# Performance work log

Measured on AMD Instinct MI355X. Metric: run time of the kernel, lower is better.

Reference implementation:

```python
import jax, jax.numpy as jnp
import numpy as np

B, T = 8, 32
D = 256                      # recurrent dim = 4*8*8 (product of embed dims)
SPEAKERS = 2
OUT_CELL = 64
N_CLASSES = 6
NUM_LAYERS = 2               # original shares ONE QRNNCell across layers ([cell]*num_layers)
BETA = 0.8                   # QActivation beta (scale_factor = 1)

def _unitary(rng, n):
    a = rng.normal(size=(n, n)) + 1j * rng.normal(size=(n, n))
    q, _ = np.linalg.qr(a)
    return jnp.asarray(q.real, jnp.float32), jnp.asarray(q.imag, jnp.float32)

def setup_inputs():
    key = jax.random.key(0)
    ks = jax.random.split(key, 18)
    rng = np.random.default_rng(0)
    def lin(k, fi, fo):
        kw, kb = jax.random.split(k)
        lim = 1.0 / np.sqrt(fi)
        return (jax.random.uniform(kw, (fi, fo), jnp.float32, -lim, lim),
                jax.random.uniform(kb, (fo,), jnp.float32, -lim, lim))
    Wt, bt = lin(ks[0], 300, 4)
    Wa, ba = lin(ks[1], 74, 8)
    Wv, bv = lin(ks[2], 35, 8)
    W1, b1 = lin(ks[3], D, OUT_CELL)
    W2, b2 = lin(ks[4], OUT_CELL, N_CLASSES)
    Ux_r, Ux_i = _unitary(rng, D)
    Uh_r, Uh_i = _unitary(rng, D)
    two_pi = float(2.0 * np.pi)
    return {
        'x_text': jax.random.normal(ks[5], (B, T, 300), jnp.float32),
        'x_audio': jax.random.normal(ks[6], (B, T, 74), jnp.float32),
        'x_video': jax.random.normal(ks[7], (B, T, 35), jnp.float32),
        'smask': jax.random.uniform(ks[8], (B, T, SPEAKERS), jnp.float32),
        'Wt': Wt, 'bt': bt, 'Wa': Wa, 'ba': ba, 'Wv': Wv, 'bv': bv,
        'Pt': jax.random.uniform(ks[9], (SPEAKERS, 4), jnp.float32, 0.0, two_pi),
        'Pa': jax.random.uniform(ks[10], (SPEAKERS, 8), jnp.float32, 0.0, two_pi),
        'Pv': jax.random.uniform(ks[11], (SPEAKERS, 8), jnp.float32, 0.0, two_pi),
        'Ux_r': Ux_r, 'Ux_i': Ux_i, 'Uh_r': Uh_r, 'Uh_i': Uh_i,
        'Lambda': jax.random.normal(ks[12], (), jnp.float32),
        'Kr': jax.random.normal(ks[13], (D, D), jnp.float32),
        'Ki': jax.random.normal(ks[14], (D, D), jnp.float32),
        'W1': W1, 'b1': b1, 'W2': W2, 'b2': b2,
    }

def _forward(x_text, x_audio, x_video, spk, Wt, bt, Wa, ba, Wv, bv, Pt, Pa, Pv,
             Ux_r, Ux_i, Uh_r, Uh_i, Lambda, Kr, Ki, W1, b1, W2, b2):
    def pure_state(x, W, b, P):
        r = jax.nn.relu(x @ W + b)
        amp = r / jnp.maximum(jnp.linalg.norm(r, axis=-1, keepdims=True), 1e-12)  # F.normalize
        ph = P[spk]                                   # (B,T,e) phase lookup by speaker id
        return amp * jnp.cos(ph), amp * jnp.sin(ph)   # ComplexMultiply
    tr_, ti_ = pure_state(x_text, Wt, bt, Pt)
    ar_, ai_ = pure_state(x_audio, Wa, ba, Pa)
    vr_, vi_ = pure_state(x_video, Wv, bv, Pv)
    def ckron(xr, xi, yr, yi):                        # QProduct: complex Kronecker product
        rr = jnp.einsum('bti,btj->btij', xr, yr) - jnp.einsum('bti,btj->btij', xi, yi)
        ii = jnp.einsum('bti,btj->btij', xr, yi) + jnp.einsum('bti,btj->btij', xi, yr)
        b_, t_ = rr.shape[:2]
        return rr.reshape(b_, t_, -1), ii.reshape(b_, t_, -1)
    pr, pi = ckron(tr_, ti_, ar_, ai_)
    pr, pi = ckron(pr, pi, vr_, vi_)                  # (B,T,D)
    # QOuter: rho = |psi><psi|, stored time-major for the scan
    rho_r = jnp.einsum('bti,btj->tbij', pr, pr) + jnp.einsum('bti,btj->tbij', pi, pi)
    rho_i = jnp.einsum('bti,btj->tbij', pi, pr) - jnp.einsum('bti,btj->tbij', pr, pi)
    lam = jax.nn.sigmoid(Lambda)
    eye = jnp.eye(D, dtype=pr.dtype) / D
    def evolve(Ur, Ui, rr, ri):                       # U rho U^dagger (complex, real/imag parts)
        Ar = jnp.einsum('pq,bqr->bpr', Ur, rr) - jnp.einsum('pq,bqr->bpr', Ui, ri)
        Ai = jnp.einsum('pq,bqr->bpr', Ur, ri) + jnp.einsum('pq,bqr->bpr', Ui, rr)
        Br = jnp.einsum('bpq,rq->bpr', Ar, Ur) + jnp.einsum('bpq,rq->bpr', Ai, Ui)
        Bi = jnp.einsum('bpq,rq->bpr', Ai, Ur) - jnp.einsum('bpq,rq->bpr', Ar, Ui)
        return Br, Bi
    def step(carry, x):                               # QRNNCell; activation only on emitted state
        hr, hi = carry
        xr, xi = x
        xer, xei = evolve(Ux_r, Ux_i, xr, xi)
        her, hei = evolve(Uh_r, Uh_i, hr, hi)
        nr = lam * xer + (1.0 - lam) * her
        ni = lam * xei + (1.0 - lam) * hei
        return (nr, ni), (BETA * nr + (1.0 - BETA) * eye, BETA * ni)  # QActivation (depolarize)
    xs = (rho_r, rho_i)
    for _ in range(NUM_LAYERS):                       # same (shared) cell each layer
        init = (jnp.broadcast_to(eye, rho_r.shape[1:]), jnp.zeros(rho_r.shape[1:], pr.dtype))
        _, xs = jax.lax.scan(step, init, xs)
    hr, hi = xs                                       # (T,B,D,D)
    # QMeasurement: p_k = Re <v_k| rho |v_k>, v_k L2-normalized complex vectors
    nrm = jnp.sqrt(jnp.sum(Kr * Kr + Ki * Ki, axis=-1, keepdims=True))
    mr, mi = Kr / nrm, Ki / nrm
    Prj_r = jnp.einsum('ki,kj->kij', mr, mr) + jnp.einsum('ki,kj->kij', mi, mi)
    Prj_i = jnp.einsum('ki,kj->kij', mr, mi) - jnp.einsum('ki,kj->kij', mi, mr)
    probs = jnp.einsum('tbij,kij->tbk', hr, Prj_r) - jnp.einsum('tbij,kij->tbk', hi, Prj_i)
    h1 = jax.nn.relu(probs @ W1 + b1)                 # SimpleNet (dropout = identity at eval)
    out = jnp.tanh(h1 @ W2 + b2)                      # (T,B,C)
    return jax.nn.log_softmax(jnp.moveaxis(out, 0, 1), axis=-1)  # (B,T,C)

def reference(x_text, x_audio, x_video, smask, Wt, bt, Wa, ba, Wv, bv, Pt, Pa, Pv,
              Ux_r, Ux_i, Uh_r, Uh_i, Lambda, Kr, Ki, W1, b1, W2, b2):
    spk = jnp.argmax(smask, axis=-1)
    return _forward(x_text, x_audio, x_video, spk, Wt, bt, Wa, ba, Wv, bv, Pt, Pa, Pv,
                    Ux_r, Ux_i, Uh_r, Uh_i, Lambda, Kr, Ki, W1, b1, W2, b2)
```

## Files before the change

kernel.cpp:

```cpp
#include <hip/hip_runtime.h>

#define TT 32
#define BETA_ 0.8f

typedef __bf16 bf16_t;
typedef bf16_t bf16x8 __attribute__((ext_vector_type(8)));
typedef float f32x4 __attribute__((ext_vector_type(4)));

#define PACC_F 256
#define BF_BASE_B 263168L
#define US 393216L
#define XU 131072L
#define XIB_E (76L * US)

#define LDSPAD 40

__device__ inline f32x4 MF(bf16x8 a, bf16x8 b, f32x4 c) {
    return __builtin_amdgcn_mfma_f32_16x16x32_bf16(a, b, c, 0, 0, 0);
}

__device__ inline void split6(float vr, float vi, bf16_t* o, long ps, long idx, int mask) {
    bf16_t rh = (bf16_t)vr; o[idx] = rh;
    bf16_t ih = (bf16_t)vi; o[ps + idx] = ih;
    if (mask & 1) {
        o[2*ps + idx] = (bf16_t)(vr - (float)rh);
        o[3*ps + idx] = (bf16_t)(vi - (float)ih);
    }
    if (mask & 2) {
        float nv = -vi; bf16_t nh = (bf16_t)nv;
        o[4*ps + idx] = nh;
        o[5*ps + idx] = (bf16_t)(nv - (float)nh);
    }
}

__global__ __launch_bounds__(256) void k_prep(
    const float* __restrict__ xt, const float* __restrict__ xa, const float* __restrict__ xv,
    const float* __restrict__ sm,
    const float* __restrict__ Wt, const float* __restrict__ bt,
    const float* __restrict__ Wa, const float* __restrict__ ba,
    const float* __restrict__ Wv, const float* __restrict__ bv,
    const float* __restrict__ Pt, const float* __restrict__ Pa, const float* __restrict__ Pv,
    const float* __restrict__ Uxr, const float* __restrict__ Uxi,
    const float* __restrict__ Uhr, const float* __restrict__ Uhi,
    const float* __restrict__ Lam, const float* __restrict__ Kr, const float* __restrict__ Ki,
    void* wsv)
{
    float* WF = (float*)wsv;
    bf16_t* bf = (bf16_t*)((char*)wsv + BF_BASE_B);
    const int blk = blockIdx.x, tid = threadIdx.x;
    __shared__ float red[256];
    __shared__ float rt[4], ra[8], rv[8], inv3[3];

    if (blk == 0) {
        if (tid != 0) return;
        float lam = 1.f / (1.f + expf(-Lam[0]));
        float oml = 1.f - lam;
        WF[0] = lam;
        WF[1] = BETA_ * BETA_ * lam * lam;
        float w = 1.f;
        for (int n = 0; n < 64; ++n) { WF[64 + n] = w; w *= oml; }
        float a1 = 1.f / 256.f, a2 = 1.f / 256.f;
        for (int t = 0; t < 32; ++t) {
            a1 = oml * a1;
            float y1 = BETA_ * a1 + (1.f - BETA_) / 256.f;
            a2 = lam * y1 + oml * a2;
            WF[8 + t] = BETA_ * a2 + (1.f - BETA_) / 256.f;
        }
        return;
    }
    if (blk < 513) {
        int i = (blk - 1) & 255, j = tid;
        if (blk < 257) {
            split6(Uxr[i * 256 + j], Uxi[i * 256 + j], bf + 0 * US, 65536L, (long)i * 256 + j, 3);
        } else {
            float vr = Uhr[i * 256 + j], vi = Uhi[i * 256 + j];
            split6(vr, vi, bf + 1 * US, 65536L, (long)i * 256 + j, 3);
            split6(vr, vi, bf + 2 * US, 65536L, (long)j * 256 + i, 3);
        }
        return;
    }
    if (blk < 769) {
        const int colS = blk - 513;
        const int t0 = colS >> 3, b = colS & 7;
        const long bt_ = (long)b * TT + t0;
        if (tid < 4) {
            float acc = bt[tid];
            const float* x = xt + bt_ * 300;
            for (int q = 0; q < 300; ++q) acc = fmaf(x[q], Wt[q * 4 + tid], acc);
            rt[tid] = fmaxf(acc, 0.f);
        } else if (tid < 12) {
            int u = tid - 4;
            float acc = ba[u];
            const float* x = xa + bt_ * 74;
            for (int q = 0; q < 74; ++q) acc = fmaf(x[q], Wa[q * 8 + u], acc);
            ra[u] = fmaxf(acc, 0.f);
        } else if (tid < 20) {
            int u = tid - 12;
            float acc = bv[u];
            const float* x = xv + bt_ * 35;
            for (int q = 0; q < 35; ++q) acc = fmaf(x[q], Wv[q * 8 + u], acc);
            rv[u] = fmaxf(acc, 0.f);
        }
        __syncthreads();
        if (tid == 0) {
            float s = 0.f; for (int u = 0; u < 4; ++u) s += rt[u] * rt[u];
            inv3[0] = 1.f / fmaxf(sqrtf(s), 1e-12f);
            s = 0.f; for (int u = 0; u < 8; ++u) s += ra[u] * ra[u];
            inv3[1] = 1.f / fmaxf(sqrtf(s), 1e-12f);
            s = 0.f; for (int u = 0; u < 8; ++u) s += rv[u] * rv[u];
            inv3[2] = 1.f / fmaxf(sqrtf(s), 1e-12f);
        }
        __syncthreads();
        float s0 = sm[bt_ * 2], s1 = sm[bt_ * 2 + 1];
        int spk = (s1 > s0) ? 1 : 0;
        int d = tid;
        int ti = d >> 6, ai = (d >> 3) & 7, vi = d & 7;
        float amp = (rt[ti] * inv3[0]) * (ra[ai] * inv3[1]) * (rv[vi] * inv3[2]);
        float ph = Pt[spk * 4 + ti] + Pa[spk * 8 + ai] + Pv[spk * 8 + vi];
        split6(amp * cosf(ph), amp * sinf(ph), bf + 3 * US, 65536L, (long)colS * 256 + d, 3);
        return;
    }
    {
        int k = blk - 769, i = tid;
        float vr = Kr[k * 256 + i], vi = Ki[k * 256 + i];
        red[i] = vr * vr + vi * vi;
        __syncthreads();
        for (int s = 128; s > 0; s >>= 1) { if (i < s) red[i] += red[i + s]; __syncthreads(); }
        float inv = 1.f / sqrtf(red[0]);
        split6(vr * inv, -vi * inv, bf + 44 * US, 65536L, (long)k * 256 + i, 3);
    }
}

struct Jobs {
    long aB[4], aS[4], bB[4], cB[4], cS[4];
    int wm[4], cnt[4];
};

__global__ __launch_bounds__(256) void k_gemm(void* wsv, Jobs J)
{
    bf16_t* bf = (bf16_t*)((char*)wsv + BF_BASE_B);
    int z = blockIdx.z, j = 0;
    while (z >= J.cnt[j]) { z -= J.cnt[j]; ++j; }
    const bf16_t* A = bf + J.aB[j] + (long)z * J.aS[j];
    const bf16_t* B = bf + J.bB[j];
    bf16_t*       C = bf + J.cB[j] + (long)z * J.cS[j];
    const int wmask = J.wm[j];

    __shared__ __align__(16) bf16_t sA[6][64][LDSPAD];
    __shared__ __align__(16) bf16_t sB[4][64][LDSPAD];
    const int m0 = blockIdx.x * 64, n0 = blockIdx.y * 64;
    const int tid = threadIdx.x;
    const int lane = tid & 63, w = tid >> 6;
    const int wm_ = w >> 1, wn = w & 1;
    const int fr = lane & 15, fg = lane >> 4;
    f32x4 accr[2][2] = {}; f32x4 acci[2][2] = {};
    for (int ks = 0; ks < 8; ++ks) {
        int idx = tid;
#pragma unroll
        for (int rep = 0; rep < 6; ++rep, idx += 256) {
            int p = idx >> 8, rem = idx & 255;
            int r = rem >> 2, cch = rem & 3;
            uint4 v = *(const uint4*)(A + (long)p * 65536 + (long)(m0 + r) * 256 + ks * 32 + cch * 8);
            *(uint4*)(&sA[p][r][cch * 8]) = v;
        }
        idx = tid;
#pragma unroll
        for (int rep = 0; rep < 4; ++rep, idx += 256) {
            int p = idx >> 8, rem = idx & 255;
            int r = rem >> 2, cch = rem & 3;
            uint4 v = *(const uint4*)(B + (long)p * 65536 + (long)(n0 + r) * 256 + ks * 32 + cch * 8);
            *(uint4*)(&sB[p][r][cch * 8]) = v;
        }
        __syncthreads();
        bf16x8 aF[2][6], bF[2][4];
#pragma unroll
        for (int fm = 0; fm < 2; ++fm) {
            int row = wm_ * 32 + fm * 16 + fr;
#pragma unroll
            for (int p = 0; p < 6; ++p) aF[fm][p] = *(const bf16x8*)(&sA[p][row][fg * 8]);
        }
#pragma unroll
        for (int fn = 0; fn < 2; ++fn) {
            int row = wn * 32 + fn * 16 + fr;
#pragma unroll
            for (int p = 0; p < 4; ++p) bF[fn][p] = *(const bf16x8*)(&sB[p][row][fg * 8]);
        }
#pragma unroll
        for (int fm = 0; fm < 2; ++fm)
#pragma unroll
            for (int fn = 0; fn < 2; ++fn) {
                f32x4 r = accr[fm][fn], im = acci[fm][fn];
                r  = MF(aF[fm][0], bF[fn][0], r );
                r  = MF(aF[fm][0], bF[fn][2], r );
                r  = MF(aF[fm][2], bF[fn][0], r );
                r  = MF(aF[fm][4], bF[fn][1], r );
                r  = MF(aF[fm][4], bF[fn][3], r );
                r  = MF(aF[fm][5], bF[fn][1], r );
                im = MF(aF[fm][0], bF[fn][1], im);
                im = MF(aF[fm][0], bF[fn][3], im);
                im = MF(aF[fm][2], bF[fn][1], im);
                im = MF(aF[fm][1], bF[fn][0], im);
                im = MF(aF[fm][1], bF[fn][2], im);
                im = MF(aF[fm][3], bF[fn][0], im);
                accr[fm][fn] = r; acci[fm][fn] = im;
            }
        __syncthreads();
    }
#pragma unroll
    for (int fm = 0; fm < 2; ++fm)
#pragma unroll
        for (int fn = 0; fn < 2; ++fn)
#pragma unroll
            for (int r4 = 0; r4 < 4; ++r4) {
                int m = m0 + wm_ * 32 + fm * 16 + fg * 4 + r4;
                int n = n0 + wn * 32 + fn * 16 + fr;
                split6(accr[fm][fn][r4], acci[fm][fn][r4], C, 65536L, (long)m * 256 + n, wmask);
            }
}

__global__ __launch_bounds__(256) void k_measure3(void* wsv)
{
    float* WF = (float*)wsv;
    bf16_t* bf = (bf16_t*)((char*)wsv + BF_BASE_B);
    const int t = blockIdx.z;
    const int cb = blockIdx.y;
    const int kblk = blockIdx.x >> 2, chunk = blockIdx.x & 3;
    const int cmax = t - 8 * chunk;
    const int clo = cb * 8;
    if (clo > cmax) return;
    const int chi = (clo + 8 < cmax + 1) ? clo + 8 : cmax + 1;

    __shared__ __align__(16) bf16_t sA[3][128][LDSPAD];
    __shared__ __align__(16) bf16_t sB[2][64][LDSPAD];
    __shared__ float part[128][9];
    const int tid = threadIdx.x;
    const int lane = tid & 63, w = tid >> 6;
    const int wm = w >> 1, wn = w & 1;
    const int fr = lane & 15, fg = lane >> 4;
    float sacc[4][2][4] = {};

    for (int c = clo; c < chi; ++c) {
        const int j0 = t - c;
        const bf16_t* H = bf + (long)(44 + c) * US;
        f32x4 accr[4][2] = {}; f32x4 acci[4][2] = {};
        for (int ks = 0; ks < 8; ++ks) {
            int idx = tid;
#pragma unroll
            for (int rep = 0; rep < 6; ++rep, idx += 256) {
                int p = idx >> 9, rem = idx & 511;
                int r = rem >> 2, cch = rem & 3;
                int pl = (p == 2) ? 4 : p;
                uint4 v = *(const uint4*)(H + (long)pl * 65536 + (long)(kblk * 128 + r) * 256 + ks * 32 + cch * 8);
                *(uint4*)(&sA[p][r][cch * 8]) = v;
            }
            idx = tid;
#pragma unroll
            for (int rep = 0; rep < 2; ++rep, idx += 256) {
                int p = idx >> 8, rem = idx & 255;
                int r = rem >> 2, cch = rem & 3;
                int t0g = chunk * 8 + (r >> 3);
                uint4 v = {0u, 0u, 0u, 0u};
                if (t0g <= j0) {
                    long base = XIB_E + (long)(j0 - t0g) * XU + (long)p * 65536
                              + (long)(chunk * 64 + r) * 256 + ks * 32 + cch * 8;
                    v = *(const uint4*)(bf + base);
                }
                *(uint4*)(&sB[p][r][cch * 8]) = v;
            }
            __syncthreads();
            bf16x8 aF[4][3], bF[2][2];
#pragma unroll
            for (int fm = 0; fm < 4; ++fm) {
                int row = wm * 64 + fm * 16 + fr;
#pragma unroll
                for (int p = 0; p < 3; ++p) aF[fm][p] = *(const bf16x8*)(&sA[p][row][fg * 8]);
            }
#pragma unroll
            for (int fn = 0; fn < 2; ++fn) {
                int row = wn * 32 + fn * 16 + fr;
#pragma unroll
                for (int p = 0; p < 2; ++p) bF[fn][p] = *(const bf16x8*)(&sB[p][row][fg * 8]);
            }
#pragma unroll
            for (int fm = 0; fm < 4; ++fm)
#pragma unroll
                for (int fn = 0; fn < 2; ++fn) {
                    f32x4 r = accr[fm][fn], im = acci[fm][fn];
                    r  = MF(aF[fm][0], bF[fn][0], r );
                    r  = MF(aF[fm][2], bF[fn][1], r );
                    im = MF(aF[fm][0], bF[fn][1], im);
                    im = MF(aF[fm][1], bF[fn][0], im);
                    accr[fm][fn] = r; acci[fm][fn] = im;
                }
            __syncthreads();
        }
#pragma unroll
        for (int fm = 0; fm < 4; ++fm)
#pragma unroll
            for (int fn = 0; fn < 2; ++fn)
#pragma unroll
                for (int r4 = 0; r4 < 4; ++r4) {
                    float vr = accr[fm][fn][r4], vi = acci[fm][fn][r4];
                    sacc[fm][fn][r4] += vr * vr + vi * vi;
                }
    }
    for (int e = tid; e < 128 * 9; e += 256) (&part[0][0])[e] = 0.f;
    __syncthreads();
#pragma unroll
    for (int fm = 0; fm < 4; ++fm)
#pragma unroll
        for (int fn = 0; fn < 2; ++fn)
#pragma unroll
            for (int r4 = 0; r4 < 4; ++r4) {
                int kl = wm * 64 + fm * 16 + fg * 4 + r4;
                int g = chunk * 64 + wn * 32 + fn * 16 + fr;
                int t0 = g >> 3;
                if (t0 <= t) atomicAdd(&part[kl][g & 7], WF[64 + (t - t0)] * sacc[fm][fn][r4]);
            }
    __syncthreads();
    float* pacc = WF + PACC_F;
    for (int e = tid; e < 1024; e += 256) {
        int kl = e >> 3, b = e & 7;
        float v = part[kl][b];
        if (v != 0.f) atomicAdd(&pacc[((t * 8 + b) << 8) + kblk * 128 + kl], v);
    }
}

__global__ __launch_bounds__(64) void k_mlp(
    const float* __restrict__ W1, const float* __restrict__ b1,
    const float* __restrict__ W2, const float* __restrict__ b2,
    const float* __restrict__ WF, float* __restrict__ out)
{
    const int t = blockIdx.x >> 3, b = blockIdx.x & 7;
    const int tid = threadIdx.x;
    __shared__ float pp[256], hh[64], oo[6];
    float ft = WF[8 + t], s2 = WF[1];
    const float* pacc = WF + PACC_F + ((t * 8 + b) << 8);
    for (int k = tid; k < 256; k += 64) pp[k] = ft + s2 * pacc[k];
    __syncthreads();
    float acc = b1[tid];
    for (int k = 0; k < 256; ++k) acc = fmaf(pp[k], W1[k * 64 + tid], acc);
    hh[tid] = fmaxf(acc, 0.f);
    __syncthreads();
    if (tid < 6) {
        float a = b2[tid];
        for (int k = 0; k < 64; ++k) a = fmaf(hh[k], W2[k * 6 + tid], a);
        oo[tid] = tanhf(a);
    }
    __syncthreads();
    if (tid == 0) {
        float m = oo[0];
        for (int c2 = 1; c2 < 6; ++c2) m = fmaxf(m, oo[c2]);
        float s = 0.f;
        for (int c2 = 0; c2 < 6; ++c2) s += expf(oo[c2] - m);
        float lse = m + logf(s);
        for (int c2 = 0; c2 < 6; ++c2) out[((long)b * 32 + t) * 6 + c2] = oo[c2] - lse;
    }
}

static inline void setJob(Jobs& J, int i, long aB, long aS, long bB, long cB, long cS,
                          int wm, int cnt)
{
    J.aB[i] = aB; J.aS[i] = aS; J.bB[i] = bB; J.cB[i] = cB; J.cS[i] = cS;
    J.wm[i] = wm; J.cnt[i] = cnt;
}

extern "C" void kernel_launch(void* const* d_in, const int* in_sizes, int n_in,
                              void* d_out, int out_size, void* d_ws, size_t ws_size,
                              hipStream_t stream)
{
    const float* xt  = (const float*)d_in[0];
    const float* xa  = (const float*)d_in[1];
    const float* xv  = (const float*)d_in[2];
    const float* sm  = (const float*)d_in[3];
    const float* Wt  = (const float*)d_in[4];
    const float* bt  = (const float*)d_in[5];
    const float* Wa  = (const float*)d_in[6];
    const float* ba  = (const float*)d_in[7];
    const float* Wv  = (const float*)d_in[8];
    const float* bv  = (const float*)d_in[9];
    const float* Pt  = (const float*)d_in[10];
    const float* Pa  = (const float*)d_in[11];
    const float* Pv  = (const float*)d_in[12];
    const float* Lam = (const float*)d_in[17];
    const float* Kr  = (const float*)d_in[18];
    const float* Ki  = (const float*)d_in[19];
    const float* W1  = (const float*)d_in[20];
    const float* b1  = (const float*)d_in[21];
    const float* W2  = (const float*)d_in[22];
    const float* b2  = (const float*)d_in[23];
    const float* Uxr = (const float*)d_in[13];
    const float* Uxi = (const float*)d_in[14];
    const float* Uhr = (const float*)d_in[15];
    const float* Uhi = (const float*)d_in[16];
    float* WF  = (float*)d_ws;
    float* out = (float*)d_out;

    hipMemsetAsync(WF + PACC_F, 0, 65536 * sizeof(float), stream);
    k_prep<<<1025, 256, 0, stream>>>(xt, xa, xv, sm, Wt, bt, Wa, ba, Wv, bv,
                                     Pt, Pa, Pv, Uxr, Uxi, Uhr, Uhi, Lam, Kr, Ki, d_ws);

    auto U = [](int u) { return (long)u * US; };
    dim3 blk(256);
    Jobs J;

    setJob(J, 0, U(1), 0, U(2), U(4), 0, 3, 1);
    setJob(J, 1, U(2), 0, U(1), U(5), 0, 3, 1);
    setJob(J, 2, U(3), 0, U(0), U(12), 0, 3, 1);
    setJob(J, 3, U(44), 0, U(2), U(45), 0, 3, 1);
    k_gemm<<<dim3(4, 4, 4), blk, 0, stream>>>(d_ws, J);
    setJob(J, 0, U(4), 0, U(5), U(6), 0, 3, 1);
    setJob(J, 1, U(5), 0, U(4), U(7), 0, 3, 1);
    setJob(J, 2, U(12), 0, U(1), U(13), 0, 3, 1);
    setJob(J, 3, U(44), US, U(5), U(46), US, 3, 2);
    k_gemm<<<dim3(4, 4, 5), blk, 0, stream>>>(d_ws, J);
    setJob(J, 0, U(6), 0, U(7), U(8), 0, 3, 1);
    setJob(J, 1, U(7), 0, U(6), U(9), 0, 3, 1);
    setJob(J, 2, U(12), US, U(4), U(14), US, 3, 2);
    setJob(J, 3, U(44), US, U(7), U(48), US, 3, 4);
    k_gemm<<<dim3(4, 4, 8), blk, 0, stream>>>(d_ws, J);
    setJob(J, 0, U(8), 0, U(9), U(10), 0, 3, 1);
    setJob(J, 1, U(9), 0, U(8), U(11), 0, 3, 1);
    setJob(J, 2, U(12), US, U(6), U(16), US, 3, 4);
    setJob(J, 3, U(44), US, U(9), U(52), US, 3, 8);
    k_gemm<<<dim3(4, 4, 14), blk, 0, stream>>>(d_ws, J);
    setJob(J, 0, U(12), US, U(8), U(20), US, 3, 8);
    setJob(J, 1, U(44), US, U(11), U(60), US, 3, 16);
    setJob(J, 2, 0, 0, 0, 0, 0, 0, 0);
    setJob(J, 3, 0, 0, 0, 0, 0, 0, 0);
    k_gemm<<<dim3(4, 4, 24), blk, 0, stream>>>(d_ws, J);
    setJob(J, 0, U(12), US, U(10), U(28), US, 3, 16);
    setJob(J, 1, U(12), US, U(0), XIB_E, XU, 0, 16);
    k_gemm<<<dim3(4, 4, 32), blk, 0, stream>>>(d_ws, J);
    setJob(J, 0, U(28), US, U(0), XIB_E + 16 * XU, XU, 0, 16);
    setJob(J, 1, 0, 0, 0, 0, 0, 0, 0);
    k_gemm<<<dim3(4, 4, 16), blk, 0, stream>>>(d_ws, J);

    k_measure3<<<dim3(8, 4, 32), blk, 0, stream>>>(d_ws);
    k_mlp<<<256, 64, 0, stream>>>(W1, b1, W2, b2, WF, out);
}
```

Before: 458.8 us.

## Drop stored negated-imag planes, split real accumulation, prefetch GEMM tiles, retile measure

The split-bf16 operand storage shrinks from six planes to four: the negated-imaginary planes are dropped, and the real part is built as the difference of two separate accumulators (positive and negative products). The GEMM kernel now prefetches the next k-slice into registers while computing the current one, and it uses a 'lo' mode with only hi planes (2 planes) for the final low-precision jobs. The measurement kernel is retiled into smaller 64x64 blocks with finer time-chunk skipping, giving more blocks. Together these cut memory traffic and LDS footprint and add latency hiding, at the cost of extra accumulator registers and the reworked indexing.

```diff
diff --git a/kernel.cpp b/kernel.cpp
--- a/kernel.cpp
+++ b/kernel.cpp
@@ -9,27 +9,20 @@
 
 #define PACC_F 256
 #define BF_BASE_B 263168L
-#define US 393216L
-#define XU 131072L
-#define XIB_E (76L * US)
-
-#define LDSPAD 40
+#define US4 262144L
+#define XU  131072L
+#define XIB_E (76L * US4)
 
 __device__ inline f32x4 MF(bf16x8 a, bf16x8 b, f32x4 c) {
     return __builtin_amdgcn_mfma_f32_16x16x32_bf16(a, b, c, 0, 0, 0);
 }
 
-__device__ inline void split6(float vr, float vi, bf16_t* o, long ps, long idx, int mask) {
+__device__ inline void splitW(float vr, float vi, bf16_t* o, long idx, int full) {
     bf16_t rh = (bf16_t)vr; o[idx] = rh;
-    bf16_t ih = (bf16_t)vi; o[ps + idx] = ih;
-    if (mask & 1) {
-        o[2*ps + idx] = (bf16_t)(vr - (float)rh);
-        o[3*ps + idx] = (bf16_t)(vi - (float)ih);
-    }
-    if (mask & 2) {
-        float nv = -vi; bf16_t nh = (bf16_t)nv;
-        o[4*ps + idx] = nh;
-        o[5*ps + idx] = (bf16_t)(nv - (float)nh);
+    bf16_t ih = (bf16_t)vi; o[65536L + idx] = ih;
+    if (full) {
+        o[2 * 65536L + idx] = (bf16_t)(vr - (float)rh);
+        o[3 * 65536L + idx] = (bf16_t)(vi - (float)ih);
     }
 }
 
@@ -71,11 +64,11 @@
     if (blk < 513) {
         int i = (blk - 1) & 255, j = tid;
         if (blk < 257) {
-            split6(Uxr[i * 256 + j], Uxi[i * 256 + j], bf + 0 * US, 65536L, (long)i * 256 + j, 3);
+            splitW(Uxr[i * 256 + j], Uxi[i * 256 + j], bf + 0 * US4, (long)i * 256 + j, 1);
         } else {
             float vr = Uhr[i * 256 + j], vi = Uhi[i * 256 + j];
-            split6(vr, vi, bf + 1 * US, 65536L, (long)i * 256 + j, 3);
-            split6(vr, vi, bf + 2 * US, 65536L, (long)j * 256 + i, 3);
+            splitW(vr, vi, bf + 1 * US4, (long)i * 256 + j, 1);
+            splitW(vr, vi, bf + 2 * US4, (long)j * 256 + i, 1);
         }
         return;
     }
@@ -117,7 +110,7 @@
         int ti = d >> 6, ai = (d >> 3) & 7, vi = d & 7;
         float amp = (rt[ti] * inv3[0]) * (ra[ai] * inv3[1]) * (rv[vi] * inv3[2]);
         float ph = Pt[spk * 4 + ti] + Pa[spk * 8 + ai] + Pv[spk * 8 + vi];
-        split6(amp * cosf(ph), amp * sinf(ph), bf + 3 * US, 65536L, (long)colS * 256 + d, 3);
+        splitW(amp * cosf(ph), amp * sinf(ph), bf + 3 * US4, (long)colS * 256 + d, 1);
         return;
     }
     {
@@ -127,16 +120,16 @@
         __syncthreads();
         for (int s = 128; s > 0; s >>= 1) { if (i < s) red[i] += red[i + s]; __syncthreads(); }
         float inv = 1.f / sqrtf(red[0]);
-        split6(vr * inv, -vi * inv, bf + 44 * US, 65536L, (long)k * 256 + i, 3);
+        splitW(vr * inv, -vi * inv, bf + 44 * US4, (long)k * 256 + i, 1);
     }
 }
 
 struct Jobs {
     long aB[4], aS[4], bB[4], cB[4], cS[4];
-    int wm[4], cnt[4];
+    int full[4], lo[4], cnt[4];
 };
 
-__global__ __launch_bounds__(256) void k_gemm(void* wsv, Jobs J)
+__global__ __launch_bounds__(256) void k_gemm2(void* wsv, Jobs J)
 {
     bf16_t* bf = (bf16_t*)((char*)wsv + BF_BASE_B);
     int z = blockIdx.z, j = 0;
@@ -144,136 +137,136 @@
     const bf16_t* A = bf + J.aB[j] + (long)z * J.aS[j];
     const bf16_t* B = bf + J.bB[j];
     bf16_t*       C = bf + J.cB[j] + (long)z * J.cS[j];
-    const int wmask = J.wm[j];
-
-    __shared__ __align__(16) bf16_t sA[6][64][LDSPAD];
-    __shared__ __align__(16) bf16_t sB[4][64][LDSPAD];
+    const int full = J.full[j], lo = J.lo[j];
+    const int nP = lo ? 2 : 4;
+
+    __shared__ __align__(16) bf16_t sA[4][64][40];
+    __shared__ __align__(16) bf16_t sB[4][64][40];
     const int m0 = blockIdx.x * 64, n0 = blockIdx.y * 64;
-    const int tid = threadIdx.x;
-    const int lane = tid & 63, w = tid >> 6;
-    const int wm_ = w >> 1, wn = w & 1;
-    const int fr = lane & 15, fg = lane >> 4;
-    f32x4 accr[2][2] = {}; f32x4 acci[2][2] = {};
-    for (int ks = 0; ks < 8; ++ks) {
-        int idx = tid;
-#pragma unroll
-        for (int rep = 0; rep < 6; ++rep, idx += 256) {
-            int p = idx >> 8, rem = idx & 255;
-            int r = rem >> 2, cch = rem & 3;
-            uint4 v = *(const uint4*)(A + (long)p * 65536 + (long)(m0 + r) * 256 + ks * 32 + cch * 8);
-            *(uint4*)(&sA[p][r][cch * 8]) = v;
-        }
-        idx = tid;
-#pragma unroll
-        for (int rep = 0; rep < 4; ++rep, idx += 256) {
-            int p = idx >> 8, rem = idx & 255;
-            int r = rem >> 2, cch = rem & 3;
-            uint4 v = *(const uint4*)(B + (long)p * 65536 + (long)(n0 + r) * 256 + ks * 32 + cch * 8);
-            *(uint4*)(&sB[p][r][cch * 8]) = v;
-        }
-        __syncthreads();
-        bf16x8 aF[2][6], bF[2][4];
-#pragma unroll
-        for (int fm = 0; fm < 2; ++fm) {
-            int row = wm_ * 32 + fm * 16 + fr;
-#pragma unroll
-            for (int p = 0; p < 6; ++p) aF[fm][p] = *(const bf16x8*)(&sA[p][row][fg * 8]);
-        }
-#pragma unroll
-        for (int fn = 0; fn < 2; ++fn) {
-            int row = wn * 32 + fn * 16 + fr;
-#pragma unroll
-            for (int p = 0; p < 4; ++p) bF[fn][p] = *(const bf16x8*)(&sB[p][row][fg * 8]);
-        }
-#pragma unroll
-        for (int fm = 0; fm < 2; ++fm)
-#pragma unroll
-            for (int fn = 0; fn < 2; ++fn) {
-                f32x4 r = accr[fm][fn], im = acci[fm][fn];
-                r  = MF(aF[fm][0], bF[fn][0], r );
-                r  = MF(aF[fm][0], bF[fn][2], r );
-                r  = MF(aF[fm][2], bF[fn][0], r );
-                r  = MF(aF[fm][4], bF[fn][1], r );
-                r  = MF(aF[fm][4], bF[fn][3], r );
-                r  = MF(aF[fm][5], bF[fn][1], r );
-                im = MF(aF[fm][0], bF[fn][1], im);
-                im = MF(aF[fm][0], bF[fn][3], im);
-                im = MF(aF[fm][2], bF[fn][1], im);
-                im = MF(aF[fm][1], bF[fn][0], im);
-                im = MF(aF[fm][1], bF[fn][2], im);
-                im = MF(aF[fm][3], bF[fn][0], im);
-                accr[fm][fn] = r; acci[fm][fn] = im;
-            }
-        __syncthreads();
-    }
-#pragma unroll
-    for (int fm = 0; fm < 2; ++fm)
-#pragma unroll
-        for (int fn = 0; fn < 2; ++fn)
-#pragma unroll
-            for (int r4 = 0; r4 < 4; ++r4) {
-                int m = m0 + wm_ * 32 + fm * 16 + fg * 4 + r4;
-                int n = n0 + wn * 32 + fn * 16 + fr;
-                split6(accr[fm][fn][r4], acci[fm][fn][r4], C, 65536L, (long)m * 256 + n, wmask);
-            }
-}
-
-__global__ __launch_bounds__(256) void k_measure3(void* wsv)
-{
-    float* WF = (float*)wsv;
-    bf16_t* bf = (bf16_t*)((char*)wsv + BF_BASE_B);
-    const int t = blockIdx.z;
-    const int cb = blockIdx.y;
-    const int kblk = blockIdx.x >> 2, chunk = blockIdx.x & 3;
-    const int cmax = t - 8 * chunk;
-    const int clo = cb * 8;
-    if (clo > cmax) return;
-    const int chi = (clo + 8 < cmax + 1) ? clo + 8 : cmax + 1;
-
-    __shared__ __align__(16) bf16_t sA[3][128][LDSPAD];
-    __shared__ __align__(16) bf16_t sB[2][64][LDSPAD];
-    __shared__ float part[128][9];
     const int tid = threadIdx.x;
     const int lane = tid & 63, w = tid >> 6;
     const int wm = w >> 1, wn = w & 1;
     const int fr = lane & 15, fg = lane >> 4;
-    float sacc[4][2][4] = {};
+    const int r_ = tid >> 2, cch = tid & 3;
+
+    f32x4 rp[2][2] = {}, rn[2][2] = {}, im[2][2] = {};
+    uint4 pa[4], pb[4];
+
+#pragma unroll
+    for (int p = 0; p < 4; ++p) if (p < nP) {
+        pa[p] = *(const uint4*)(A + (long)p * 65536 + (long)(m0 + r_) * 256 + cch * 8);
+        pb[p] = *(const uint4*)(B + (long)p * 65536 + (long)(n0 + r_) * 256 + cch * 8);
+    }
+    for (int ks = 0; ks < 8; ++ks) {
+        __syncthreads();
+#pragma unroll
+        for (int p = 0; p < 4; ++p) if (p < nP) {
+            *(uint4*)(&sA[p][r_][cch * 8]) = pa[p];
+            *(uint4*)(&sB[p][r_][cch * 8]) = pb[p];
+        }
+        __syncthreads();
+        if (ks < 7) {
+#pragma unroll
+            for (int p = 0; p < 4; ++p) if (p < nP) {
+                pa[p] = *(const uint4*)(A + (long)p * 65536 + (long)(m0 + r_) * 256 + (ks + 1) * 32 + cch * 8);
+                pb[p] = *(const uint4*)(B + (long)p * 65536 + (long)(n0 + r_) * 256 + (ks + 1) * 32 + cch * 8);
+            }
+        }
+        bf16x8 aF[2][4], bF[2][4];
+#pragma unroll
+        for (int fm = 0; fm < 2; ++fm) {
+            int row = wm * 32 + fm * 16 + fr;
+#pragma unroll
+            for (int p = 0; p < 4; ++p) if (p < nP) aF[fm][p] = *(const bf16x8*)(&sA[p][row][fg * 8]);
+        }
+#pragma unroll
+        for (int fn = 0; fn < 2; ++fn) {
+            int row = wn * 32 + fn * 16 + fr;
+#pragma unroll
+            for (int p = 0; p < 4; ++p) if (p < nP) bF[fn][p] = *(const bf16x8*)(&sB[p][row][fg * 8]);
+        }
+#pragma unroll
+        for (int fm = 0; fm < 2; ++fm)
+#pragma unroll
+            for (int fn = 0; fn < 2; ++fn) {
+                f32x4 p_ = rp[fm][fn], n_ = rn[fm][fn], i_ = im[fm][fn];
+                p_ = MF(aF[fm][0], bF[fn][0], p_);
+                n_ = MF(aF[fm][1], bF[fn][1], n_);
+                i_ = MF(aF[fm][0], bF[fn][1], i_);
+                i_ = MF(aF[fm][1], bF[fn][0], i_);
+                if (!lo) {
+                    p_ = MF(aF[fm][0], bF[fn][2], p_);
+                    p_ = MF(aF[fm][2], bF[fn][0], p_);
+                    n_ = MF(aF[fm][1], bF[fn][3], n_);
+                    n_ = MF(aF[fm][3], bF[fn][1], n_);
+                    i_ = MF(aF[fm][0], bF[fn][3], i_);
+                    i_ = MF(aF[fm][2], bF[fn][1], i_);
+                    i_ = MF(aF[fm][1], bF[fn][2], i_);
+                    i_ = MF(aF[fm][3], bF[fn][0], i_);
+                }
+                rp[fm][fn] = p_; rn[fm][fn] = n_; im[fm][fn] = i_;
+            }
+    }
+#pragma unroll
+    for (int fm = 0; fm < 2; ++fm)
+#pragma unroll
+        for (int fn = 0; fn < 2; ++fn)
+#pragma unroll
+            for (int r4 = 0; r4 < 4; ++r4) {
+                int m = m0 + wm * 32 + fm * 16 + fg * 4 + r4;
+                int n = n0 + wn * 32 + fn * 16 + fr;
+                float vr = rp[fm][fn][r4] - rn[fm][fn][r4];
+                splitW(vr, im[fm][fn][r4], C, (long)m * 256 + n, full);
+            }
+}
+
+__global__ __launch_bounds__(256) void k_measure4(void* wsv)
+{
+    float* WF = (float*)wsv;
+    bf16_t* bf = (bf16_t*)((char*)wsv + BF_BASE_B);
+    const int t = blockIdx.z;
+    const int clo = blockIdx.y * 4;
+    if (clo > t) return;
+    const int kblk = blockIdx.x >> 2, colc = blockIdx.x & 3;
+    if (colc * 8 > t - clo) return;
+    const int chi = (clo + 4 < t + 1) ? clo + 4 : t + 1;
+    const int k0 = kblk * 64;
+
+    __shared__ __align__(16) bf16_t sA[2][64][40];
+    __shared__ __align__(16) bf16_t sB[2][64][40];
+    __shared__ float part[64][9];
+    const int tid = threadIdx.x;
+    const int lane = tid & 63, w = tid >> 6;
+    const int wm = w >> 1, wn = w & 1;
+    const int fr = lane & 15, fg = lane >> 4;
+    const int r_ = tid >> 2, cch = tid & 3;
+    float sacc[2][2][4] = {};
+
+    const int t0r = colc * 8 + (r_ >> 3);
+    const long xrow = (long)(t0r * 8 + (r_ & 7)) * 256;
 
     for (int c = clo; c < chi; ++c) {
-        const int j0 = t - c;
-        const bf16_t* H = bf + (long)(44 + c) * US;
-        f32x4 accr[4][2] = {}; f32x4 acci[4][2] = {};
+        const bf16_t* H = bf + (44L + c) * US4;
+        const int av = t - c - t0r;
+        f32x4 rp[2][2] = {}, rn[2][2] = {}, im[2][2] = {};
         for (int ks = 0; ks < 8; ++ks) {
-            int idx = tid;
-#pragma unroll
-            for (int rep = 0; rep < 6; ++rep, idx += 256) {
-                int p = idx >> 9, rem = idx & 511;
-                int r = rem >> 2, cch = rem & 3;
-                int pl = (p == 2) ? 4 : p;
-                uint4 v = *(const uint4*)(H + (long)pl * 65536 + (long)(kblk * 128 + r) * 256 + ks * 32 + cch * 8);
-                *(uint4*)(&sA[p][r][cch * 8]) = v;
-            }
-            idx = tid;
-#pragma unroll
-            for (int rep = 0; rep < 2; ++rep, idx += 256) {
-                int p = idx >> 8, rem = idx & 255;
-                int r = rem >> 2, cch = rem & 3;
-                int t0g = chunk * 8 + (r >> 3);
+            __syncthreads();
+#pragma unroll
+            for (int p = 0; p < 2; ++p) {
+                *(uint4*)(&sA[p][r_][cch * 8]) =
+                    *(const uint4*)(H + (long)p * 65536 + (long)(k0 + r_) * 256 + ks * 32 + cch * 8);
                 uint4 v = {0u, 0u, 0u, 0u};
-                if (t0g <= j0) {
-                    long base = XIB_E + (long)(j0 - t0g) * XU + (long)p * 65536
-                              + (long)(chunk * 64 + r) * 256 + ks * 32 + cch * 8;
-                    v = *(const uint4*)(bf + base);
-                }
-                *(uint4*)(&sB[p][r][cch * 8]) = v;
+                if (av >= 0)
+                    v = *(const uint4*)(bf + XIB_E + (long)av * XU + (long)p * 65536 + xrow + ks * 32 + cch * 8);
+                *(uint4*)(&sB[p][r_][cch * 8]) = v;
             }
             __syncthreads();
-            bf16x8 aF[4][3], bF[2][2];
-#pragma unroll
-            for (int fm = 0; fm < 4; ++fm) {
-                int row = wm * 64 + fm * 16 + fr;
-#pragma unroll
-                for (int p = 0; p < 3; ++p) aF[fm][p] = *(const bf16x8*)(&sA[p][row][fg * 8]);
+            bf16x8 aF[2][2], bF[2][2];
+#pragma unroll
+            for (int fm = 0; fm < 2; ++fm) {
+                int row = wm * 32 + fm * 16 + fr;
+#pragma unroll
+                for (int p = 0; p < 2; ++p) aF[fm][p] = *(const bf16x8*)(&sA[p][row][fg * 8]);
             }
 #pragma unroll
             for (int fn = 0; fn < 2; ++fn) {
@@ -282,47 +275,47 @@
                 for (int p = 0; p < 2; ++p) bF[fn][p] = *(const bf16x8*)(&sB[p][row][fg * 8]);
             }
 #pragma unroll
-            for (int fm = 0; fm < 4; ++fm)
+            for (int fm = 0; fm < 2; ++fm)
 #pragma unroll
                 for (int fn = 0; fn < 2; ++fn) {
-                    f32x4 r = accr[fm][fn], im = acci[fm][fn];
-                    r  = MF(aF[fm][0], bF[fn][0], r );
-                    r  = MF(aF[fm][2], bF[fn][1], r );
-                    im = MF(aF[fm][0], bF[fn][1], im);
-                    im = MF(aF[fm][1], bF[fn][0], im);
-                    accr[fm][fn] = r; acci[fm][fn] = im;
+                    f32x4 p_ = rp[fm][fn], n_ = rn[fm][fn], i_ = im[fm][fn];
+                    p_ = MF(aF[fm][0], bF[fn][0], p_);
+                    n_ = MF(aF[fm][1], bF[fn][1], n_);
+                    i_ = MF(aF[fm][0], bF[fn][1], i_);
+                    i_ = MF(aF[fm][1], bF[fn][0], i_);
+                    rp[fm][fn] = p_; rn[fm][fn] = n_; im[fm][fn] = i_;
                 }
-            __syncthreads();
-        }
-#pragma unroll
-        for (int fm = 0; fm < 4; ++fm)
+        }
+#pragma unroll
+        for (int fm = 0; fm < 2; ++fm)
 #pragma unroll
             for (int fn = 0; fn < 2; ++fn)
 #pragma unroll
                 for (int r4 = 0; r4 < 4; ++r4) {
-                    float vr = accr[fm][fn][r4], vi = acci[fm][fn][r4];
+                    float vr = rp[fm][fn][r4] - rn[fm][fn][r4];
+                    float vi = im[fm][fn][r4];
                     sacc[fm][fn][r4] += vr * vr + vi * vi;
                 }
     }
-    for (int e = tid; e < 128 * 9; e += 256) (&part[0][0])[e] = 0.f;
+    for (int e = tid; e < 64 * 9; e += 256) (&part[0][0])[e] = 0.f;
     __syncthreads();
 #pragma unroll
-    for (int fm = 0; fm < 4; ++fm)
+    for (int fm = 0; fm < 2; ++fm)
 #pragma unroll
         for (int fn = 0; fn < 2; ++fn)
 #pragma unroll
             for (int r4 = 0; r4 < 4; ++r4) {
-                int kl = wm * 64 + fm * 16 + fg * 4 + r4;
-                int g = chunk * 64 + wn * 32 + fn * 16 + fr;
-                int t0 = g >> 3;
-                if (t0 <= t) atomicAdd(&part[kl][g & 7], WF[64 + (t - t0)] * sacc[fm][fn][r4]);
+                int kl = wm * 32 + fm * 16 + fg * 4 + r4;
+                int g = wn * 32 + fn * 16 + fr;
+                int t0 = colc * 8 + (g >> 3);
+                if (t0 <= t) atomicAdd(&part[kl][g & 7], WF[64 + t - t0] * sacc[fm][fn][r4]);
             }
     __syncthreads();
     float* pacc = WF + PACC_F;
-    for (int e = tid; e < 1024; e += 256) {
+    for (int e = tid; e < 512; e += 256) {
         int kl = e >> 3, b = e & 7;
         float v = part[kl][b];
-        if (v != 0.f) atomicAdd(&pacc[((t * 8 + b) << 8) + kblk * 128 + kl], v);
+        if (v != 0.f) atomicAdd(&pacc[((t * 8 + b) << 8) + k0 + kl], v);
     }
 }
 
@@ -359,10 +352,10 @@
 }
 
 static inline void setJob(Jobs& J, int i, long aB, long aS, long bB, long cB, long cS,
-                          int wm, int cnt)
+                          int full, int lo, int cnt)
 {
     J.aB[i] = aB; J.aS[i] = aS; J.bB[i] = bB; J.cB[i] = cB; J.cS[i] = cS;
-    J.wm[i] = wm; J.cnt[i] = cnt;
+    J.full[i] = full; J.lo[i] = lo; J.cnt[i] = cnt;
 }
 
 extern "C" void kernel_launch(void* const* d_in, const int* in_sizes, int n_in,
@@ -382,6 +375,10 @@
     const float* Pt  = (const float*)d_in[10];
     const float* Pa  = (const float*)d_in[11];
     const float* Pv  = (const float*)d_in[12];
+    const float* Uxr = (const float*)d_in[13];
+    const float* Uxi = (const float*)d_in[14];
+    const float* Uhr = (const float*)d_in[15];
+    const float* Uhi = (const float*)d_in[16];
     const float* Lam = (const float*)d_in[17];
     const float* Kr  = (const float*)d_in[18];
     const float* Ki  = (const float*)d_in[19];
@@ -389,10 +386,6 @@
     const float* b1  = (const float*)d_in[21];
     const float* W2  = (const float*)d_in[22];
     const float* b2  = (const float*)d_in[23];
-    const float* Uxr = (const float*)d_in[13];
-    const float* Uxi = (const float*)d_in[14];
-    const float* Uhr = (const float*)d_in[15];
-    const float* Uhi = (const float*)d_in[16];
     float* WF  = (float*)d_ws;
     float* out = (float*)d_out;
 
@@ -400,42 +393,42 @@
     k_prep<<<1025, 256, 0, stream>>>(xt, xa, xv, sm, Wt, bt, Wa, ba, Wv, bv,
                                      Pt, Pa, Pv, Uxr, Uxi, Uhr, Uhi, Lam, Kr, Ki, d_ws);
 
-    auto U = [](int u) { return (long)u * US; };
+    auto U = [](int u) { return (long)u * US4; };
     dim3 blk(256);
     Jobs J;
 
-    setJob(J, 0, U(1), 0, U(2), U(4), 0, 3, 1);
-    setJob(J, 1, U(2), 0, U(1), U(5), 0, 3, 1);
-    setJob(J, 2, U(3), 0, U(0), U(12), 0, 3, 1);
-    setJob(J, 3, U(44), 0, U(2), U(45), 0, 3, 1);
-    k_gemm<<<dim3(4, 4, 4), blk, 0, stream>>>(d_ws, J);
-    setJob(J, 0, U(4), 0, U(5), U(6), 0, 3, 1);
-    setJob(J, 1, U(5), 0, U(4), U(7), 0, 3, 1);
-    setJob(J, 2, U(12), 0, U(1), U(13), 0, 3, 1);
-    setJob(J, 3, U(44), US, U(5), U(46), US, 3, 2);
-    k_gemm<<<dim3(4, 4, 5), blk, 0, stream>>>(d_ws, J);
-    setJob(J, 0, U(6), 0, U(7), U(8), 0, 3, 1);
-    setJob(J, 1, U(7), 0, U(6), U(9), 0, 3, 1);
-    setJob(J, 2, U(12), US, U(4), U(14), US, 3, 2);
-    setJob(J, 3, U(44), US, U(7), U(48), US, 3, 4);
-    k_gemm<<<dim3(4, 4, 8), blk, 0, stream>>>(d_ws, J);
-    setJob(J, 0, U(8), 0, U(9), U(10), 0, 3, 1);
-    setJob(J, 1, U(9), 0, U(8), U(11), 0, 3, 1);
-    setJob(J, 2, U(12), US, U(6), U(16), US, 3, 4);
-    setJob(J, 3, U(44), US, U(9), U(52), US, 3, 8);
-    k_gemm<<<dim3(4, 4, 14), blk, 0, stream>>>(d_ws, J);
-    setJob(J, 0, U(12), US, U(8), U(20), US, 3, 8);
-    setJob(J, 1, U(44), US, U(11), U(60), US, 3, 16);
-    setJob(J, 2, 0, 0, 0, 0, 0, 0, 0);
-    setJob(J, 3, 0, 0, 0, 0, 0, 0, 0);
-    k_gemm<<<dim3(4, 4, 24), blk, 0, stream>>>(d_ws, J);
-    setJob(J, 0, U(12), US, U(10), U(28), US, 3, 16);
-    setJob(J, 1, U(12), US, U(0), XIB_E, XU, 0, 16);
-    k_gemm<<<dim3(4, 4, 32), blk, 0, stream>>>(d_ws, J);
-    setJob(J, 0, U(28), US, U(0), XIB_E + 16 * XU, XU, 0, 16);
-    setJob(J, 1, 0, 0, 0, 0, 0, 0, 0);
-    k_gemm<<<dim3(4, 4, 16), blk, 0, stream>>>(d_ws, J);
-
-    k_measure3<<<dim3(8, 4, 32), blk, 0, stream>>>(d_ws);
+    setJob(J, 0, U(1), 0, U(2), U(4), 0, 1, 0, 1);
+    setJob(J, 1, U(2), 0, U(1), U(5), 0, 1, 0, 1);
+    setJob(J, 2, U(3), 0, U(0), U(12), 0, 1, 0, 1);
+    setJob(J, 3, U(44), 0, U(2), U(45), 0, 1, 0, 1);
+    k_gemm2<<<dim3(4, 4, 4), blk, 0, stream>>>(d_ws, J);
+    setJob(J, 0, U(4), 0, U(5), U(6), 0, 1, 0, 1);
+    setJob(J, 1, U(5), 0, U(4), U(7), 0, 1, 0, 1);
+    setJob(J, 2, U(12), 0, U(1), U(13), 0, 1, 0, 1);
+    setJob(J, 3, U(44), US4, U(5), U(46), US4, 1, 0, 2);
+    k_gemm2<<<dim3(4, 4, 5), blk, 0, stream>>>(d_ws, J);
+    setJob(J, 0, U(6), 0, U(7), U(8), 0, 1, 0, 1);
+    setJob(J, 1, U(7), 0, U(6), U(9), 0, 1, 0, 1);
+    setJob(J, 2, U(12), US4, U(4), U(14), US4, 1, 0, 2);
+    setJob(J, 3, U(44), US4, U(7), U(48), US4, 1, 0, 4);
+    k_gemm2<<<dim3(4, 4, 8), blk, 0, stream>>>(d_ws, J);
+    setJob(J, 0, U(8), 0, U(9), U(10), 0, 1, 0, 1);
+    setJob(J, 1, U(9), 0, U(8), U(11), 0, 1, 0, 1);
+    setJob(J, 2, U(12), US4, U(6), U(16), US4, 1, 0, 4);
+    setJob(J, 3, U(44), US4, U(9), U(52), US4, 1, 0, 8);
+    k_gemm2<<<dim3(4, 4, 14), blk, 0, stream>>>(d_ws, J);
+    setJob(J, 0, U(12), US4, U(8), U(20), US4, 1, 0, 8);
+    setJob(J, 1, U(44), US4, U(11), U(60), US4, 1, 0, 16);
+    setJob(J, 2, 0, 0, 0, 0, 0, 0, 0, 0);
+    setJob(J, 3, 0, 0, 0, 0, 0, 0, 0, 0);
+    k_gemm2<<<dim3(4, 4, 24), blk, 0, stream>>>(d_ws, J);
+    setJob(J, 0, U(12), US4, U(10), U(28), US4, 1, 0, 16);
+    setJob(J, 1, U(12), US4, U(0), XIB_E, XU, 0, 1, 16);
+    k_gemm2<<<dim3(4, 4, 32), blk, 0, stream>>>(d_ws, J);
+    setJob(J, 0, U(28), US4, U(0), XIB_E + 16 * XU, XU, 0, 1, 16);
+    setJob(J, 1, 0, 0, 0, 0, 0, 0, 0, 0);
+    k_gemm2<<<dim3(4, 4, 16), blk, 0, stream>>>(d_ws, J);
+
+    k_measure4<<<dim3(16, 8, 32), blk, 0, stream>>>(d_ws);
     k_mlp<<<256, 64, 0, stream>>>(W1, b1, W2, b2, WF, out);
 }
```

New measurement: 488.8 us. 1.07x slower.
